# Kernel tuning notes

Measured on AMD Instinct MI355X. Metric: run time of the kernel, lower is better.

Reference implementation:

```python
import jax, jax.numpy as jnp
import numpy as np

SPATIAL = [(100, 100), (50, 50), (25, 25), (13, 13)]
NUM_POINTS = [4, 4, 4, 4]
N_HEADS = 8
HIDDEN = 256
OFFSET_SCALE = 0.5

B, Q = 16, 300
S = sum(h * w for h, w in SPATIAL)


def setup_inputs() -> dict:
    key = jax.random.key(0)
    ks = jax.random.split(key, 7)
    total_points = N_HEADS * sum(NUM_POINTS)  # 128
    return {
        "hidden_states": jax.random.normal(ks[0], (B, Q, HIDDEN), jnp.float32),
        "encoder_hidden_states": jax.random.normal(ks[1], (B, S, HIDDEN), jnp.float32),
        "reference_points": jax.random.uniform(ks[2], (B, Q, 1, 4), jnp.float32),
        "W_off": jax.random.normal(ks[3], (HIDDEN, total_points * 2), jnp.float32) * 0.02,
        "b_off": jnp.zeros((total_points * 2,), jnp.float32),
        "W_attn": jax.random.normal(ks[4], (HIDDEN, total_points), jnp.float32) * 0.02,
        "b_attn": jnp.zeros((total_points,), jnp.float32),
    }


def _bilinear_sample(img, x, y, h, w):
    # img: [B, H, h, w, D]; x, y: [B, Q, H, P] pixel coords (align_corners=False)
    x0 = jnp.floor(x)
    y0 = jnp.floor(y)
    wx1 = x - x0
    wx0 = 1.0 - wx1
    wy1 = y - y0
    wy0 = 1.0 - wy1

    bi = jnp.arange(img.shape[0])[:, None, None, None]
    hi = jnp.arange(img.shape[1])[None, None, :, None]

    def gather(yy, xx):
        valid = (xx >= 0) & (xx <= w - 1) & (yy >= 0) & (yy <= h - 1)
        xi = jnp.clip(xx, 0, w - 1).astype(jnp.int32)
        yi = jnp.clip(yy, 0, h - 1).astype(jnp.int32)
        v = img[bi, hi, yi, xi]  # [B, Q, H, P, D]
        return v * valid[..., None].astype(img.dtype)

    return (gather(y0, x0) * (wy0 * wx0)[..., None]
            + gather(y0, x0 + 1) * (wy0 * wx1)[..., None]
            + gather(y0 + 1, x0) * (wy1 * wx0)[..., None]
            + gather(y0 + 1, x0 + 1) * (wy1 * wx1)[..., None])


def reference(hidden_states, encoder_hidden_states, reference_points, W_off, b_off, W_attn, b_attn):
    b, q, _ = hidden_states.shape
    s = encoder_hidden_states.shape[1]
    d = HIDDEN // N_HEADS
    p_total = sum(NUM_POINTS)

    # sampling offsets and attention weights projections
    off = (hidden_states @ W_off + b_off).reshape(b, q, N_HEADS, p_total, 2)
    aw = (hidden_states @ W_attn + b_attn).reshape(b, q, N_HEADS, p_total)
    aw = jax.nn.softmax(aw, axis=-1)

    # reference_points last dim == 4 branch
    scale = jnp.concatenate([jnp.full((n,), 1.0 / n, jnp.float32) for n in NUM_POINTS])
    offset = off * scale[:, None] * reference_points[..., 2:][:, :, :, None, :] * OFFSET_SCALE
    loc = reference_points[..., :2][:, :, :, None, :] + offset  # [B, Q, H, P, 2] in [0,1]

    value = encoder_hidden_states.reshape(b, s, N_HEADS, d)

    outs = []
    start, pstart = 0, 0
    for (h, w), n in zip(SPATIAL, NUM_POINTS):
        sz = h * w
        v = value[:, start:start + sz].reshape(b, h, w, N_HEADS, d).transpose(0, 3, 1, 2, 4)
        l = loc[:, :, :, pstart:pstart + n, :]
        # grid_sample align_corners=False: x = ((2*loc-1+1)*W - 1)/2 = loc*W - 0.5
        x = l[..., 0] * w - 0.5
        y = l[..., 1] * h - 0.5
        outs.append(_bilinear_sample(v, x, y, h, w))
        start += sz
        pstart += n

    sampled = jnp.concatenate(outs, axis=3)  # [B, Q, H, P_total, D]
    out = jnp.einsum('bqhpd,bqhp->bqhd', sampled, aw).reshape(b, q, HIDDEN)
    return out, aw
```

## Files before the change

kernel.cpp:

```cpp
#include <hip/hip_runtime.h>
#include <hip/hip_bf16.h>

#define B_      16
#define Q_      300
#define BQ      (B_*Q_)
#define HIDDEN_ 256
#define NHEADS  8
#define PTOT    16
#define S_      13294
#define NOFF    256
#define NATTN   128
#define NCOLS   (NOFF+NATTN)
#define OSTRIDE 388
#define AS      264

typedef __attribute__((ext_vector_type(8))) short bf16x8;
typedef __attribute__((ext_vector_type(4))) float floatx4;

__device__ __forceinline__ short f2bf(float f) {
    unsigned u = __float_as_uint(f);
    unsigned r = (u + 0x7fffu + ((u >> 16) & 1u)) >> 16;
    return (short)r;
}

__global__ __launch_bounds__(256) void prep_kernel(
    const float* __restrict__ W_off,
    const float* __restrict__ W_attn,
    short* __restrict__ Wt)
{
    int id = blockIdx.x * 256 + threadIdx.x;
    int j = id >> 8;
    int k = id & 255;
    float v = (j < NOFF) ? W_off[k * NOFF + j] : W_attn[k * NATTN + (j - NOFF)];
    Wt[id] = f2bf(v);
}

__global__ __launch_bounds__(512) void proj_kernel(
    const float* __restrict__ hidden,
    const float* __restrict__ refp,
    const short* __restrict__ Wt,
    const float* __restrict__ b_off,
    const float* __restrict__ b_attn,
    float* __restrict__ aw_out,
    float* __restrict__ loc_out)
{
    __shared__ short A_s[16 * AS];
    __shared__ float o_s[16 * OSTRIDE];

    const int tid  = threadIdx.x;
    const int wave = tid >> 6;
    const int lane = tid & 63;
    const int m    = lane & 15;
    const int quad = lane >> 4;
    const int row0 = blockIdx.x * 16;

    {
        const int r  = tid >> 5;
        const int ks = (tid & 31) * 8;
        const float* hp = hidden + (size_t)(row0 + r) * HIDDEN_ + ks;
        float4 a0 = *(const float4*)hp;
        float4 a1 = *(const float4*)(hp + 4);
        bf16x8 v;
        v[0] = f2bf(a0.x); v[1] = f2bf(a0.y); v[2] = f2bf(a0.z); v[3] = f2bf(a0.w);
        v[4] = f2bf(a1.x); v[5] = f2bf(a1.y); v[6] = f2bf(a1.z); v[7] = f2bf(a1.w);
        *(bf16x8*)(A_s + r * AS + ks) = v;
    }
    __syncthreads();

    floatx4 acc[3];
    #pragma unroll
    for (int i = 0; i < 3; ++i)
        #pragma unroll
        for (int r = 0; r < 4; ++r) acc[i][r] = 0.f;

    #pragma unroll
    for (int k0 = 0; k0 < HIDDEN_; k0 += 32) {
        const int kk = k0 + quad * 8;
        bf16x8 af = *(const bf16x8*)(A_s + m * AS + kk);
        #pragma unroll
        for (int i = 0; i < 3; ++i) {
            const int n0 = (wave * 3 + i) * 16;
            bf16x8 bf = *(const bf16x8*)(Wt + (size_t)(n0 + m) * HIDDEN_ + kk);
            acc[i] = __builtin_amdgcn_mfma_f32_16x16x32_bf16(af, bf, acc[i], 0, 0, 0);
        }
    }

    #pragma unroll
    for (int i = 0; i < 3; ++i) {
        const int n0  = (wave * 3 + i) * 16;
        const int col = n0 + m;
        const float bias = (col < NOFF) ? b_off[col] : b_attn[col - NOFF];
        #pragma unroll
        for (int r = 0; r < 4; ++r)
            o_s[(quad * 4 + r) * OSTRIDE + col] = acc[i][r] + bias;
    }
    __syncthreads();

    if (tid < 16 * NHEADS) {
        const int r  = tid >> 3;
        const int hd = tid & 7;
        const int row = row0 + r;

        float a[PTOT];
        float mx = -1e30f;
        #pragma unroll
        for (int p = 0; p < PTOT; ++p) {
            a[p] = o_s[r * OSTRIDE + NOFF + hd * PTOT + p];
            mx = fmaxf(mx, a[p]);
        }
        float s = 0.f;
        #pragma unroll
        for (int p = 0; p < PTOT; ++p) { a[p] = __expf(a[p] - mx); s += a[p]; }
        const float inv = 1.f / s;

        const float4 rp = ((const float4*)refp)[row];
        const float sx = 0.25f * rp.z * 0.5f;
        const float sy = 0.25f * rp.w * 0.5f;

        #pragma unroll
        for (int p = 0; p < PTOT; ++p) {
            const float awv = a[p] * inv;
            aw_out[row * NATTN + hd * PTOT + p] = awv;
            const float ox = o_s[r * OSTRIDE + (hd * PTOT + p) * 2];
            const float oy = o_s[r * OSTRIDE + (hd * PTOT + p) * 2 + 1];
            ((float2*)loc_out)[(row * NHEADS + hd) * PTOT + p] =
                make_float2(rp.x + ox * sx, rp.y + oy * sy);
        }
    }
}

__global__ __launch_bounds__(256) void sample_kernel(
    const float* __restrict__ enc,
    const float* __restrict__ aw,
    const float* __restrict__ loc,
    float* __restrict__ out)
{
    const int xcd = blockIdx.x & 7;
    const int idx = blockIdx.x >> 3;
    const int hi  = (idx >= 75);
    const int bb  = xcd * 2 + hi;
    const int qb  = idx - hi * 75;
    const int bq0 = bb * Q_ + qb * 4;

    __shared__ float2 tw_s[4 * NHEADS * PTOT * 4];

    const int tid = threadIdx.x;

    for (int t = tid; t < 4 * NHEADS * PTOT; t += 256) {
        const int g    = t >> 7;
        const int rest = t & 127;
        const int p    = rest & 15;
        const int bq   = bq0 + g;

        const float2 lxy = ((const float2*)loc)[(size_t)bq * NATTN + rest];
        const float  a   = aw[(size_t)bq * NATTN + rest];

        const int lvl   = p >> 2;
        const int Wl    = (lvl == 0) ? 100 : (lvl == 1) ? 50 : (lvl == 2) ? 25 : 13;
        const int start = (lvl == 0) ? 0 : (lvl == 1) ? 10000 : (lvl == 2) ? 12500 : 13125;

        const float x = lxy.x * (float)Wl - 0.5f;
        const float y = lxy.y * (float)Wl - 0.5f;
        const float x0f = floorf(x), y0f = floorf(y);
        const float wx1 = x - x0f, wx0 = 1.f - wx1;
        const float wy1 = y - y0f, wy0 = 1.f - wy1;
        const int x0 = (int)x0f, y0 = (int)y0f;
        const int x1 = x0 + 1,  y1 = y0 + 1;

        const int x0c = x0 < 0 ? 0 : (x0 > Wl-1 ? Wl-1 : x0);
        const int x1c = x1 < 0 ? 0 : (x1 > Wl-1 ? Wl-1 : x1);
        const int y0c = y0 < 0 ? 0 : (y0 > Wl-1 ? Wl-1 : y0);
        const int y1c = y1 < 0 ? 0 : (y1 > Wl-1 ? Wl-1 : y1);
        const bool vx0 = (x0 >= 0) & (x0 <= Wl-1);
        const bool vx1 = (x1 >= 0) & (x1 <= Wl-1);
        const bool vy0 = (y0 >= 0) & (y0 <= Wl-1);
        const bool vy1 = (y1 >= 0) & (y1 <= Wl-1);

        const int r00 = start + y0c * Wl + x0c;
        const int r01 = start + y0c * Wl + x1c;
        const int r10 = start + y1c * Wl + x0c;
        const int r11 = start + y1c * Wl + x1c;

        float2* dst = &tw_s[t * 4];
        dst[0] = make_float2(__int_as_float(r00), (vy0 & vx0) ? a * wy0 * wx0 : 0.f);
        dst[1] = make_float2(__int_as_float(r01), (vy0 & vx1) ? a * wy0 * wx1 : 0.f);
        dst[2] = make_float2(__int_as_float(r10), (vy1 & vx0) ? a * wy1 * wx0 : 0.f);
        dst[3] = make_float2(__int_as_float(r11), (vy1 & vx1) ? a * wy1 * wx1 : 0.f);
    }
    __syncthreads();

    const int g    = tid >> 6;
    const int lane = tid & 63;
    const int hd   = lane >> 3;
    const int cq   = lane & 7;
    const int bq   = bq0 + g;

    const float4* encb = (const float4*)(enc + (size_t)bb * S_ * HIDDEN_);
    const int c4   = hd * 8 + cq;
    const int base = (g * NHEADS + hd) * PTOT * 4;

    float4 acc = make_float4(0.f, 0.f, 0.f, 0.f);

    #pragma unroll 16
    for (int i = 0; i < PTOT * 4; ++i) {
        const float2 tw = tw_s[base + i];
        const int row = __float_as_int(tw.x);
        const float w = tw.y;
        const float4 v = encb[(size_t)row * 64 + c4];
        acc.x = fmaf(w, v.x, acc.x);
        acc.y = fmaf(w, v.y, acc.y);
        acc.z = fmaf(w, v.z, acc.z);
        acc.w = fmaf(w, v.w, acc.w);
    }

    ((float4*)out)[(size_t)bq * 64 + c4] = acc;
}

extern "C" void kernel_launch(void* const* d_in, const int* in_sizes, int n_in,
                              void* d_out, int out_size, void* d_ws, size_t ws_size,
                              hipStream_t stream) {
    const float* hidden = (const float*)d_in[0];
    const float* enc    = (const float*)d_in[1];
    const float* refp   = (const float*)d_in[2];
    const float* W_off  = (const float*)d_in[3];
    const float* b_off  = (const float*)d_in[4];
    const float* W_attn = (const float*)d_in[5];
    const float* b_attn = (const float*)d_in[6];

    float* out    = (float*)d_out;
    float* aw_out = out + (size_t)BQ * HIDDEN_;

    short* Wt     = (short*)d_ws;
    float* loc_ws = (float*)d_ws + 65536;

    prep_kernel<<<NCOLS * HIDDEN_ / 256, 256, 0, stream>>>(W_off, W_attn, Wt);
    proj_kernel<<<BQ / 16, 512, 0, stream>>>(hidden, refp, Wt, b_off, b_attn, aw_out, loc_ws);
    sample_kernel<<<BQ / 4, 256, 0, stream>>>(enc, aw_out, loc_ws, out);
}
```

Measured before the change: 307.8 us.

## Fuse projection, softmax and bilinear sampling into one kernel

Merges the projection/softmax kernel and the sampling kernel into a single kernel that handles 8 queries per block. It computes softmax and sampling locations per point in parallel and builds the gather tables directly in shared memory, so the loc workspace no longer takes a global round trip and one launch is removed. In exchange, the MFMA tile of 16 rows is half padded with zeros, so half of the projection compute is wasted. The XCD-aware block-to-batch mapping of the old sampler is also dropped, which may hurt L2 locality for the encoder gathers.

```diff
diff --git a/kernel.cpp b/kernel.cpp
--- a/kernel.cpp
+++ b/kernel.cpp
@@ -13,6 +13,8 @@
 #define NCOLS   (NOFF+NATTN)
 #define OSTRIDE 388
 #define AS      264
+#define MQ      8
+#define TS      68
 
 typedef __attribute__((ext_vector_type(8))) short bf16x8;
 typedef __attribute__((ext_vector_type(4))) float floatx4;
@@ -35,132 +37,111 @@
     Wt[id] = f2bf(v);
 }
 
-__global__ __launch_bounds__(512) void proj_kernel(
+__global__ __launch_bounds__(512) void fused_kernel(
     const float* __restrict__ hidden,
     const float* __restrict__ refp,
     const short* __restrict__ Wt,
     const float* __restrict__ b_off,
     const float* __restrict__ b_attn,
-    float* __restrict__ aw_out,
-    float* __restrict__ loc_out)
+    const float* __restrict__ enc,
+    float* __restrict__ out,
+    float* __restrict__ aw_out)
 {
-    __shared__ short A_s[16 * AS];
-    __shared__ float o_s[16 * OSTRIDE];
+    __shared__ float o_s[MQ * OSTRIDE];
+    __shared__ int   row_s[MQ * NHEADS * TS];
+    __shared__ float w_s[MQ * NHEADS * TS];
+
+    short* A_s = (short*)row_s;
 
     const int tid  = threadIdx.x;
-    const int wave = tid >> 6;
-    const int lane = tid & 63;
-    const int m    = lane & 15;
-    const int quad = lane >> 4;
-    const int row0 = blockIdx.x * 16;
+    const int row0 = blockIdx.x * MQ;
 
     {
         const int r  = tid >> 5;
         const int ks = (tid & 31) * 8;
-        const float* hp = hidden + (size_t)(row0 + r) * HIDDEN_ + ks;
-        float4 a0 = *(const float4*)hp;
-        float4 a1 = *(const float4*)(hp + 4);
         bf16x8 v;
-        v[0] = f2bf(a0.x); v[1] = f2bf(a0.y); v[2] = f2bf(a0.z); v[3] = f2bf(a0.w);
-        v[4] = f2bf(a1.x); v[5] = f2bf(a1.y); v[6] = f2bf(a1.z); v[7] = f2bf(a1.w);
+        if (r < MQ) {
+            const float* hp = hidden + (size_t)(row0 + r) * HIDDEN_ + ks;
+            float4 a0 = *(const float4*)hp;
+            float4 a1 = *(const float4*)(hp + 4);
+            v[0] = f2bf(a0.x); v[1] = f2bf(a0.y); v[2] = f2bf(a0.z); v[3] = f2bf(a0.w);
+            v[4] = f2bf(a1.x); v[5] = f2bf(a1.y); v[6] = f2bf(a1.z); v[7] = f2bf(a1.w);
+        } else {
+            v = (bf16x8)0;
+        }
         *(bf16x8*)(A_s + r * AS + ks) = v;
     }
     __syncthreads();
 
-    floatx4 acc[3];
+    {
+        const int wave = tid >> 6;
+        const int lane = tid & 63;
+        const int m    = lane & 15;
+        const int quad = lane >> 4;
+
+        floatx4 acc[3];
+        #pragma unroll
+        for (int i = 0; i < 3; ++i)
+            #pragma unroll
+            for (int r = 0; r < 4; ++r) acc[i][r] = 0.f;
+
+        #pragma unroll
+        for (int k0 = 0; k0 < HIDDEN_; k0 += 32) {
+            const int kk = k0 + quad * 8;
+            bf16x8 af = *(const bf16x8*)(A_s + m * AS + kk);
+            #pragma unroll
+            for (int i = 0; i < 3; ++i) {
+                const int n0 = (wave * 3 + i) * 16;
+                bf16x8 bf = *(const bf16x8*)(Wt + (size_t)(n0 + m) * HIDDEN_ + kk);
+                acc[i] = __builtin_amdgcn_mfma_f32_16x16x32_bf16(af, bf, acc[i], 0, 0, 0);
+            }
+        }
+        __syncthreads();
+
+        if (quad < 2) {
+            #pragma unroll
+            for (int i = 0; i < 3; ++i) {
+                const int col = (wave * 3 + i) * 16 + m;
+                const float bias = (col < NOFF) ? b_off[col] : b_attn[col - NOFF];
+                #pragma unroll
+                for (int r = 0; r < 4; ++r)
+                    o_s[(quad * 4 + r) * OSTRIDE + col] = acc[i][r] + bias;
+            }
+        }
+    }
+    __syncthreads();
+
     #pragma unroll
-    for (int i = 0; i < 3; ++i)
-        #pragma unroll
-        for (int r = 0; r < 4; ++r) acc[i][r] = 0.f;
-
-    #pragma unroll
-    for (int k0 = 0; k0 < HIDDEN_; k0 += 32) {
-        const int kk = k0 + quad * 8;
-        bf16x8 af = *(const bf16x8*)(A_s + m * AS + kk);
-        #pragma unroll
-        for (int i = 0; i < 3; ++i) {
-            const int n0 = (wave * 3 + i) * 16;
-            bf16x8 bf = *(const bf16x8*)(Wt + (size_t)(n0 + m) * HIDDEN_ + kk);
-            acc[i] = __builtin_amdgcn_mfma_f32_16x16x32_bf16(af, bf, acc[i], 0, 0, 0);
-        }
-    }
-
-    #pragma unroll
-    for (int i = 0; i < 3; ++i) {
-        const int n0  = (wave * 3 + i) * 16;
-        const int col = n0 + m;
-        const float bias = (col < NOFF) ? b_off[col] : b_attn[col - NOFF];
-        #pragma unroll
-        for (int r = 0; r < 4; ++r)
-            o_s[(quad * 4 + r) * OSTRIDE + col] = acc[i][r] + bias;
-    }
-    __syncthreads();
-
-    if (tid < 16 * NHEADS) {
-        const int r  = tid >> 3;
-        const int hd = tid & 7;
+    for (int half = 0; half < 2; ++half) {
+        const int t  = tid + half * 512;
+        const int r  = t >> 7;
+        const int hd = (t >> 4) & 7;
+        const int p  = t & 15;
         const int row = row0 + r;
 
-        float a[PTOT];
+        const float* lg = &o_s[r * OSTRIDE + NOFF + hd * PTOT];
         float mx = -1e30f;
         #pragma unroll
-        for (int p = 0; p < PTOT; ++p) {
-            a[p] = o_s[r * OSTRIDE + NOFF + hd * PTOT + p];
-            mx = fmaxf(mx, a[p]);
-        }
-        float s = 0.f;
-        #pragma unroll
-        for (int p = 0; p < PTOT; ++p) { a[p] = __expf(a[p] - mx); s += a[p]; }
-        const float inv = 1.f / s;
+        for (int q = 0; q < PTOT; ++q) mx = fmaxf(mx, lg[q]);
+        float sum = 0.f;
+        #pragma unroll
+        for (int q = 0; q < PTOT; ++q) sum += __expf(lg[q] - mx);
+        const float awv = __expf(lg[p] - mx) / sum;
+
+        aw_out[(size_t)row * NATTN + hd * PTOT + p] = awv;
 
         const float4 rp = ((const float4*)refp)[row];
-        const float sx = 0.25f * rp.z * 0.5f;
-        const float sy = 0.25f * rp.w * 0.5f;
-
-        #pragma unroll
-        for (int p = 0; p < PTOT; ++p) {
-            const float awv = a[p] * inv;
-            aw_out[row * NATTN + hd * PTOT + p] = awv;
-            const float ox = o_s[r * OSTRIDE + (hd * PTOT + p) * 2];
-            const float oy = o_s[r * OSTRIDE + (hd * PTOT + p) * 2 + 1];
-            ((float2*)loc_out)[(row * NHEADS + hd) * PTOT + p] =
-                make_float2(rp.x + ox * sx, rp.y + oy * sy);
-        }
-    }
-}
-
-__global__ __launch_bounds__(256) void sample_kernel(
-    const float* __restrict__ enc,
-    const float* __restrict__ aw,
-    const float* __restrict__ loc,
-    float* __restrict__ out)
-{
-    const int xcd = blockIdx.x & 7;
-    const int idx = blockIdx.x >> 3;
-    const int hi  = (idx >= 75);
-    const int bb  = xcd * 2 + hi;
-    const int qb  = idx - hi * 75;
-    const int bq0 = bb * Q_ + qb * 4;
-
-    __shared__ float2 tw_s[4 * NHEADS * PTOT * 4];
-
-    const int tid = threadIdx.x;
-
-    for (int t = tid; t < 4 * NHEADS * PTOT; t += 256) {
-        const int g    = t >> 7;
-        const int rest = t & 127;
-        const int p    = rest & 15;
-        const int bq   = bq0 + g;
-
-        const float2 lxy = ((const float2*)loc)[(size_t)bq * NATTN + rest];
-        const float  a   = aw[(size_t)bq * NATTN + rest];
+        const float ox = o_s[r * OSTRIDE + (hd * PTOT + p) * 2];
+        const float oy = o_s[r * OSTRIDE + (hd * PTOT + p) * 2 + 1];
+        const float lx = rp.x + ox * (0.125f * rp.z);
+        const float ly = rp.y + oy * (0.125f * rp.w);
 
         const int lvl   = p >> 2;
         const int Wl    = (lvl == 0) ? 100 : (lvl == 1) ? 50 : (lvl == 2) ? 25 : 13;
         const int start = (lvl == 0) ? 0 : (lvl == 1) ? 10000 : (lvl == 2) ? 12500 : 13125;
 
-        const float x = lxy.x * (float)Wl - 0.5f;
-        const float y = lxy.y * (float)Wl - 0.5f;
+        const float x = lx * (float)Wl - 0.5f;
+        const float y = ly * (float)Wl - 0.5f;
         const float x0f = floorf(x), y0f = floorf(y);
         const float wx1 = x - x0f, wx0 = 1.f - wx1;
         const float wy1 = y - y0f, wy0 = 1.f - wy1;
@@ -176,44 +157,46 @@
         const bool vy0 = (y0 >= 0) & (y0 <= Wl-1);
         const bool vy1 = (y1 >= 0) & (y1 <= Wl-1);
 
-        const int r00 = start + y0c * Wl + x0c;
-        const int r01 = start + y0c * Wl + x1c;
-        const int r10 = start + y1c * Wl + x0c;
-        const int r11 = start + y1c * Wl + x1c;
-
-        float2* dst = &tw_s[t * 4];
-        dst[0] = make_float2(__int_as_float(r00), (vy0 & vx0) ? a * wy0 * wx0 : 0.f);
-        dst[1] = make_float2(__int_as_float(r01), (vy0 & vx1) ? a * wy0 * wx1 : 0.f);
-        dst[2] = make_float2(__int_as_float(r10), (vy1 & vx0) ? a * wy1 * wx0 : 0.f);
-        dst[3] = make_float2(__int_as_float(r11), (vy1 & vx1) ? a * wy1 * wx1 : 0.f);
+        const int col  = r * NHEADS + hd;
+        const int base = col * TS + p * 4;
+        row_s[base + 0] = start + y0c * Wl + x0c;
+        row_s[base + 1] = start + y0c * Wl + x1c;
+        row_s[base + 2] = start + y1c * Wl + x0c;
+        row_s[base + 3] = start + y1c * Wl + x1c;
+        w_s[base + 0] = (vy0 & vx0) ? awv * wy0 * wx0 : 0.f;
+        w_s[base + 1] = (vy0 & vx1) ? awv * wy0 * wx1 : 0.f;
+        w_s[base + 2] = (vy1 & vx0) ? awv * wy1 * wx0 : 0.f;
+        w_s[base + 3] = (vy1 & vx1) ? awv * wy1 * wx1 : 0.f;
     }
     __syncthreads();
 
-    const int g    = tid >> 6;
-    const int lane = tid & 63;
-    const int hd   = lane >> 3;
-    const int cq   = lane & 7;
-    const int bq   = bq0 + g;
-
-    const float4* encb = (const float4*)(enc + (size_t)bb * S_ * HIDDEN_);
-    const int c4   = hd * 8 + cq;
-    const int base = (g * NHEADS + hd) * PTOT * 4;
-
-    float4 acc = make_float4(0.f, 0.f, 0.f, 0.f);
-
-    #pragma unroll 16
-    for (int i = 0; i < PTOT * 4; ++i) {
-        const float2 tw = tw_s[base + i];
-        const int row = __float_as_int(tw.x);
-        const float w = tw.y;
-        const float4 v = encb[(size_t)row * 64 + c4];
-        acc.x = fmaf(w, v.x, acc.x);
-        acc.y = fmaf(w, v.y, acc.y);
-        acc.z = fmaf(w, v.z, acc.z);
-        acc.w = fmaf(w, v.w, acc.w);
-    }
-
-    ((float4*)out)[(size_t)bq * 64 + c4] = acc;
+    {
+        const int g    = tid >> 6;
+        const int lane = tid & 63;
+        const int hd   = lane >> 3;
+        const int cq   = lane & 7;
+        const int bq   = row0 + g;
+        const int b    = bq / Q_;
+
+        const float4* encb = (const float4*)(enc + (size_t)b * S_ * HIDDEN_);
+        const int c4   = hd * 8 + cq;
+        const int base = (g * NHEADS + hd) * TS;
+
+        float4 acc = make_float4(0.f, 0.f, 0.f, 0.f);
+
+        #pragma unroll 16
+        for (int j = 0; j < PTOT * 4; ++j) {
+            const int   row = row_s[base + j];
+            const float w   = w_s[base + j];
+            const float4 v  = encb[(size_t)row * 64 + c4];
+            acc.x = fmaf(w, v.x, acc.x);
+            acc.y = fmaf(w, v.y, acc.y);
+            acc.z = fmaf(w, v.z, acc.z);
+            acc.w = fmaf(w, v.w, acc.w);
+        }
+
+        ((float4*)out)[(size_t)bq * 64 + c4] = acc;
+    }
 }
 
 extern "C" void kernel_launch(void* const* d_in, const int* in_sizes, int n_in,
@@ -230,10 +213,9 @@
     float* out    = (float*)d_out;
     float* aw_out = out + (size_t)BQ * HIDDEN_;
 
-    short* Wt     = (short*)d_ws;
-    float* loc_ws = (float*)d_ws + 65536;
+    short* Wt = (short*)d_ws;
 
     prep_kernel<<<NCOLS * HIDDEN_ / 256, 256, 0, stream>>>(W_off, W_attn, Wt);
-    proj_kernel<<<BQ / 16, 512, 0, stream>>>(hidden, refp, Wt, b_off, b_attn, aw_out, loc_ws);
-    sample_kernel<<<BQ / 4, 256, 0, stream>>>(enc, aw_out, loc_ws, out);
-}
+    fused_kernel<<<BQ / MQ, 512, 0, stream>>>(hidden, refp, Wt, b_off, b_attn,
+                                              enc, out, aw_out);
+}
```

Result: no change. 309.4 us (+0.5%).
